# Kernel tuning notes

Hardware: AMD Instinct MI355X
Metric: run time of the kernel (lower is better)

## Reference

```python
import math
import jax, jax.numpy as jnp
import numpy as np

B, S, D_MODEL, N_HEADS, D_KV = 8, 1024, 1024, 16, 64
INNER = N_HEADS * D_KV
NUM_BUCKETS, MAX_DISTANCE = 32, 128


def _relative_position_bucket(relative_position, bidirectional=True,
                              num_buckets=NUM_BUCKETS, max_distance=MAX_DISTANCE):
    # Faithful port of T5Attention._relative_position_bucket (int math).
    relative_buckets = jnp.zeros_like(relative_position)
    if bidirectional:
        num_buckets //= 2
        relative_buckets += (relative_position > 0).astype(jnp.int32) * num_buckets
        relative_position = jnp.abs(relative_position)
    else:
        relative_position = -jnp.minimum(relative_position, 0)
    max_exact = num_buckets // 2
    is_small = relative_position < max_exact
    # clamp to >=1 before log to avoid -inf -> int cast (value unused when is_small)
    rp_f = jnp.maximum(relative_position, 1).astype(jnp.float32)
    rel_if_large = max_exact + (
        jnp.log(rp_f / max_exact) / math.log(max_distance / max_exact)
        * (num_buckets - max_exact)
    ).astype(jnp.int32)
    rel_if_large = jnp.minimum(rel_if_large, num_buckets - 1)
    relative_buckets += jnp.where(is_small, relative_position, rel_if_large)
    return relative_buckets


def compute_bias(rel_bias_emb, query_length, key_length):
    context_position = jnp.arange(query_length, dtype=jnp.int32)[:, None]
    memory_position = jnp.arange(key_length, dtype=jnp.int32)[None, :]
    relative_position = memory_position - context_position  # [Q, K]
    buckets = _relative_position_bucket(relative_position, bidirectional=True)
    values = rel_bias_emb[buckets]                 # [Q, K, H]
    return jnp.transpose(values, (2, 0, 1))[None]  # [1, H, Q, K]


def setup_inputs() -> dict:
    key = jax.random.key(0)
    k1, k2, k3, k4 = jax.random.split(key, 4)
    return {
        "hidden_states": jax.random.normal(k1, (B, S, D_MODEL), jnp.float32),
        "w_qkv": jax.random.normal(k2, (3 * INNER, D_MODEL), jnp.float32) * 0.02,
        "rel_bias_emb": jax.random.normal(k3, (NUM_BUCKETS, N_HEADS), jnp.float32) * 0.02,
        "w_out": jax.random.normal(k4, (D_MODEL, INNER), jnp.float32) * 0.02,
    }


def reference(hidden_states, w_qkv, rel_bias_emb, w_out):
    # QKV projection (no bias)
    qkv = jnp.einsum('bsd,ed->bse', hidden_states, w_qkv)  # [B,S,3*INNER]
    q, k, v = jnp.split(qkv, 3, axis=-1)
    q = q.reshape(B, S, N_HEADS, D_KV)
    k = k.reshape(B, S, N_HEADS, D_KV)
    v = v.reshape(B, S, N_HEADS, D_KV)
    # T5 attention uses scale = 1.0 (no 1/sqrt(d))
    scores = jnp.einsum('bqhd,bkhd->bhqk', q, k)           # [B,H,S,S]
    scores = scores + compute_bias(rel_bias_emb, S, S)     # additive rel-pos bias
    probs = jax.nn.softmax(scores, axis=-1)
    attn = jnp.einsum('bhqk,bkhd->bqhd', probs, v).reshape(B, S, INNER)
    return jnp.einsum('bsi,di->bsd', attn, w_out)          # out_proj, no bias
```

## Files before the change

### kernel.cpp

```cpp
#include <hip/hip_runtime.h>
#include <math.h>

typedef __attribute__((ext_vector_type(8))) short short8;
typedef __attribute__((ext_vector_type(4))) float f32x4;
typedef __attribute__((ext_vector_type(16))) float f32x16;
typedef __attribute__((ext_vector_type(4))) int int32x4;
typedef unsigned short bf16_t;

#define GLOAD_LDS16(g, l)                                                   \
    __builtin_amdgcn_global_load_lds(                                       \
        (__attribute__((address_space(1))) void*)(g),                       \
        (__attribute__((address_space(3))) void*)(l), 16, 0, 0)

__device__ __forceinline__ bf16_t f2b_rne(float f) {
    unsigned int u = __float_as_uint(f);
    u += 0x7FFFu + ((u >> 16) & 1u);
    return (bf16_t)(u >> 16);
}

__device__ __forceinline__ void store_out(bf16_t* p, float v) { *p = f2b_rne(v); }
__device__ __forceinline__ void store_out(float* p, float v) { *p = v; }

__global__ __launch_bounds__(256) void f2b_kernel(const float* __restrict__ in,
                                                  bf16_t* __restrict__ out, int n4) {
    int stride = gridDim.x * 256;
    for (int i = blockIdx.x * 256 + threadIdx.x; i < n4; i += stride) {
        float4 v = ((const float4*)in)[i];
        ushort4 p;
        p.x = f2b_rne(v.x); p.y = f2b_rne(v.y);
        p.z = f2b_rne(v.z); p.w = f2b_rne(v.w);
        ((ushort4*)out)[i] = p;
    }
}

__global__ void build_bias_tab(const float* __restrict__ emb, float* __restrict__ tab) {
    int idx = blockIdx.x * 256 + threadIdx.x;
    if (idx >= 2047) return;
    int rel = idx - 1023;
    int rb = rel > 0 ? 16 : 0;
    int rp = rel < 0 ? -rel : rel;
    int bucket;
    if (rp < 8) {
        bucket = rb + rp;
    } else {
        float t = logf((float)rp * 0.125f);
        int vi = 8 + (int)(t / 2.772588722239781f * 8.0f);
        bucket = rb + (vi < 15 ? vi : 15);
    }
    #pragma unroll
    for (int hh = 0; hh < 16; hh++)
        tab[hh * 2048 + idx] = emb[bucket * 16 + hh];
}

template <typename OT>
__global__ __launch_bounds__(256) void gemm_mfma(const bf16_t* __restrict__ A,
                                                 const bf16_t* __restrict__ B,
                                                 OT* __restrict__ C, int N, int gx) {
    __shared__ __align__(16) bf16_t As[128 * 32];
    __shared__ __align__(16) bf16_t Bs[128 * 32];
    const int nwg = gridDim.x;
    const int cpx = nwg >> 3;
    const int swz = (blockIdx.x & 7) * cpx + (blockIdx.x >> 3);
    const int bx = swz % gx, by = swz / gx;

    const int tid = threadIdx.x;
    const int lane = tid & 63;
    const int wv = tid >> 6;
    const int wr = wv >> 1, wc = wv & 1;
    const int m0 = by * 128, n0 = bx * 128;
    const int cc = lane & 15, cg = lane >> 4;

    f32x4 acc[4][4];
    #pragma unroll
    for (int i = 0; i < 4; i++)
        #pragma unroll
        for (int j = 0; j < 4; j++) acc[i][j] = {0.f, 0.f, 0.f, 0.f};

    for (int k0 = 0; k0 < 1024; k0 += 32) {
        __syncthreads();
        #pragma unroll
        for (int it = 0; it < 2; it++) {
            int c = it * 256 + tid;
            int r = c >> 2, kc = (c & 3) * 8;
            GLOAD_LDS16(A + (size_t)(m0 + r) * 1024 + k0 + kc, &As[c * 8]);
            GLOAD_LDS16(B + (size_t)(n0 + r) * 1024 + k0 + kc, &Bs[c * 8]);
        }
        __syncthreads();

        short8 af[4], bf[4];
        #pragma unroll
        for (int mf = 0; mf < 4; mf++)
            af[mf] = *(const short8*)&As[(wr * 64 + mf * 16 + cc) * 32 + cg * 8];
        #pragma unroll
        for (int nf = 0; nf < 4; nf++)
            bf[nf] = *(const short8*)&Bs[(wc * 64 + nf * 16 + cc) * 32 + cg * 8];
        #pragma unroll
        for (int mf = 0; mf < 4; mf++)
            #pragma unroll
            for (int nf = 0; nf < 4; nf++)
                acc[mf][nf] = __builtin_amdgcn_mfma_f32_16x16x32_bf16(
                    af[mf], bf[nf], acc[mf][nf], 0, 0, 0);
    }

    #pragma unroll
    for (int mf = 0; mf < 4; mf++)
        #pragma unroll
        for (int j = 0; j < 4; j++) {
            size_t row = (size_t)(m0 + wr * 64 + mf * 16 + cg * 4 + j);
            OT* cp = C + row * N + n0 + wc * 64 + cc;
            #pragma unroll
            for (int nf = 0; nf < 4; nf++) store_out(cp + nf * 16, acc[mf][nf][j]);
        }
}

__global__ __launch_bounds__(256) void relayout_k(const bf16_t* __restrict__ qkvb,
                                                  bf16_t* __restrict__ klin) {
    int gid = blockIdx.x * 256 + threadIdx.x;
    int lane = gid & 63;
    int s = (gid >> 6) & 3;
    int kt = (gid >> 8) & 31;
    int bh = gid >> 13;
    int b = bh >> 4, h = bh & 15;
    int key = kt * 32 + (lane & 31);
    int d0 = 16 * s + 8 * (lane >> 5);
    const bf16_t* src = qkvb + (size_t)(b * 1024 + key) * 3072 + 1024 + h * 64 + d0;
    *(short8*)(klin + (size_t)gid * 8) = *(const short8*)src;
}

__global__ __launch_bounds__(256) void relayout_v(const bf16_t* __restrict__ qkvb,
                                                  bf16_t* __restrict__ vt2) {
    int gid = blockIdx.x * 256 + threadIdx.x;
    int lane = gid & 63;
    int i = (gid >> 6) & 3;
    int kt = (gid >> 8) & 31;
    int bh = gid >> 13;
    int b = bh >> 4, h = bh & 15;
    int half = i >> 1, s2 = i & 1;
    int key0 = kt * 32 + 16 * s2 + 8 * (lane >> 5);
    int d = (lane & 31) + 32 * half;
    const bf16_t* src = qkvb + (size_t)(b * 1024 + key0) * 3072 + 2048 + h * 64 + d;
    short8 v;
    #pragma unroll
    for (int j = 0; j < 8; j++) v[j] = (short)src[(size_t)j * 3072];
    *(short8*)(vt2 + (size_t)gid * 8) = v;
}

__global__ __launch_bounds__(256, 3) void attn_mfma4(const bf16_t* __restrict__ qkv,
                                                     const float* __restrict__ tab,
                                                     const bf16_t* __restrict__ klin,
                                                     const bf16_t* __restrict__ vt2,
                                                     bf16_t* __restrict__ attn_out) {
    __shared__ float bias2[2304];
    __shared__ bf16_t Ol[4 * 32 * 68];

    const int i = blockIdx.x;
    const int g = ((i >> 6) << 3) + (i & 7);
    const int qc = (i >> 3) & 7;
    const int b = g >> 4, h = g & 15;
    const int q0 = qc * 128;

    const int tid = threadIdx.x;
    const int lane = tid & 63;
    const int w = tid >> 6;
    const int l31 = lane & 31;
    const int hi = lane >> 5;

    const float* tabh = tab + h * 2048;
    const int wbase = 896 - q0;
    #pragma unroll
    for (int it = 0; it < 5; it++) {
        int j = it * 256 + tid;
        if (j < 1151) {
            bias2[2 * j]     = tabh[wbase + j];
            bias2[2 * j + 1] = tabh[wbase + j + 1];
        }
    }

    const size_t rs = 3072;
    const bf16_t* Qg = qkv + (size_t)b * 1024 * rs + h * 64;
    const bf16_t* kl = klin + (size_t)g * 65536;
    const bf16_t* vl = vt2 + (size_t)g * 65536;

    const int qloc = w * 32 + l31;
    short8 qf[4];
    #pragma unroll
    for (int s = 0; s < 4; s++)
        qf[s] = *(const short8*)(Qg + (size_t)(q0 + qloc) * rs + 8 * hi + 16 * s);

    f32x16 O0 = (f32x16)0.f, O1 = (f32x16)0.f;
    float m_run = -1e30f, l_run = 0.f;

    auto loadk = [&](short8 (&dst)[4], int kt) {
        const bf16_t* kp = kl + (size_t)kt * 2048 + lane * 8;
        #pragma unroll
        for (int s = 0; s < 4; s++) dst[s] = *(const short8*)(kp + s * 512);
    };

    auto compute = [&](short8 (&kf)[4], int kt) {
        const int k0 = kt * 32;
        const bf16_t* vp = vl + (size_t)kt * 2048 + lane * 8;
        short8 vf0 = *(const short8*)vp;
        short8 vf1 = *(const short8*)(vp + 512);
        short8 vf2 = *(const short8*)(vp + 1024);
        short8 vf3 = *(const short8*)(vp + 1536);

        f32x16 S = (f32x16)0.f;
        #pragma unroll
        for (int s = 0; s < 4; s++)
            S = __builtin_amdgcn_mfma_f32_32x32x16_bf16(kf[s], qf[s], S, 0, 0, 0);

        float p[16];
        #pragma unroll
        for (int gg = 0; gg < 4; gg++) {
            int bi = k0 + 8 * gg + 4 * hi + 127 - qloc;
            float2 b0 = *(const float2*)&bias2[2 * bi];
            float2 b1 = *(const float2*)&bias2[2 * (bi + 2)];
            p[4 * gg + 0] = S[4 * gg + 0] + b0.x;
            p[4 * gg + 1] = S[4 * gg + 1] + b0.y;
            p[4 * gg + 2] = S[4 * gg + 2] + b1.x;
            p[4 * gg + 3] = S[4 * gg + 3] + b1.y;
        }

        float pmax = p[0];
        #pragma unroll
        for (int r = 1; r < 16; r++) pmax = fmaxf(pmax, p[r]);
        pmax = fmaxf(pmax, __shfl_xor(pmax, 32));
        if (!__all(pmax - m_run <= 8.f)) {
            float mn = fmaxf(m_run, pmax);
            float sc = __expf(m_run - mn);
            l_run *= sc;
            #pragma unroll
            for (int r = 0; r < 16; r++) { O0[r] *= sc; O1[r] *= sc; }
            m_run = mn;
        }
        float rsum = 0.f;
        #pragma unroll
        for (int r = 0; r < 16; r++) { p[r] = __expf(p[r] - m_run); rsum += p[r]; }
        rsum += __shfl_xor(rsum, 32);
        l_run += rsum;

        unsigned int wv[8];
        #pragma unroll
        for (int ii = 0; ii < 8; ii++) {
            unsigned int t;
            asm("v_cvt_pk_bf16_f32 %0, %1, %2" : "=v"(t) : "v"(p[2 * ii]), "v"(p[2 * ii + 1]));
            wv[ii] = t;
        }
        unsigned int x0 = __shfl_xor(hi ? wv[0] : wv[2], 32);
        unsigned int x1 = __shfl_xor(hi ? wv[1] : wv[3], 32);
        unsigned int x2 = __shfl_xor(hi ? wv[4] : wv[6], 32);
        unsigned int x3 = __shfl_xor(hi ? wv[5] : wv[7], 32);
        int32x4 pf0i, pf1i;
        if (hi) {
            pf0i = (int32x4){(int)x0, (int)x1, (int)wv[2], (int)wv[3]};
            pf1i = (int32x4){(int)x2, (int)x3, (int)wv[6], (int)wv[7]};
        } else {
            pf0i = (int32x4){(int)wv[0], (int)wv[1], (int)x0, (int)x1};
            pf1i = (int32x4){(int)wv[4], (int)wv[5], (int)x2, (int)x3};
        }
        short8 pf0 = __builtin_bit_cast(short8, pf0i);
        short8 pf1 = __builtin_bit_cast(short8, pf1i);

        O0 = __builtin_amdgcn_mfma_f32_32x32x16_bf16(vf0, pf0, O0, 0, 0, 0);
        O0 = __builtin_amdgcn_mfma_f32_32x32x16_bf16(vf1, pf1, O0, 0, 0, 0);
        O1 = __builtin_amdgcn_mfma_f32_32x32x16_bf16(vf2, pf0, O1, 0, 0, 0);
        O1 = __builtin_amdgcn_mfma_f32_32x32x16_bf16(vf3, pf1, O1, 0, 0, 0);
    };

    __syncthreads();

    short8 kA[4], kB[4];
    loadk(kA, 0);
    for (int kt = 0; kt < 32; kt += 2) {
        loadk(kB, kt + 1);
        compute(kA, kt);
        if (kt < 30) loadk(kA, kt + 2);
        compute(kB, kt + 1);
    }

    float inv = 1.f / l_run;
    bf16_t* olw = &Ol[w * 32 * 68];
    #pragma unroll
    for (int r = 0; r < 16; r++) {
        int dr = (r & 3) + 8 * (r >> 2) + 4 * hi;
        olw[l31 * 68 + dr]      = f2b_rne(O0[r] * inv);
        olw[l31 * 68 + dr + 32] = f2b_rne(O1[r] * inv);
    }
    bf16_t* outp = attn_out + (size_t)(b * 1024 + q0 + w * 32) * 1024 + h * 64;
    #pragma unroll 4
    for (int i2 = 0; i2 < 32; i2++)
        outp[(size_t)i2 * 1024 + lane] = olw[i2 * 68 + lane];
}

extern "C" void kernel_launch(void* const* d_in, const int* in_sizes, int n_in,
                              void* d_out, int out_size, void* d_ws, size_t ws_size,
                              hipStream_t stream) {
    const float* hs   = (const float*)d_in[0];
    const float* wqkv = (const float*)d_in[1];
    const float* emb  = (const float*)d_in[2];
    const float* wout = (const float*)d_in[3];
    float* out = (float*)d_out;

    char* p = (char*)d_ws;
    bf16_t* qkvb  = (bf16_t*)p; p += (size_t)8192 * 3072 * 2;
    bf16_t* attnb = (bf16_t*)p; p += (size_t)8192 * 1024 * 2;
    bf16_t* hsb   = (bf16_t*)p; p += (size_t)8192 * 1024 * 2;
    bf16_t* wqkvb = (bf16_t*)p; p += (size_t)3072 * 1024 * 2;
    bf16_t* woutb = (bf16_t*)p; p += (size_t)1024 * 1024 * 2;
    bf16_t* klin  = (bf16_t*)p; p += (size_t)128 * 65536 * 2;
    bf16_t* vt2   = (bf16_t*)p; p += (size_t)128 * 65536 * 2;
    float*  tab   = (float*)p;

    f2b_kernel<<<2048, 256, 0, stream>>>(hs, hsb, 8192 * 1024 / 4);
    f2b_kernel<<<768, 256, 0, stream>>>(wqkv, wqkvb, 3072 * 1024 / 4);
    f2b_kernel<<<256, 256, 0, stream>>>(wout, woutb, 1024 * 1024 / 4);
    build_bias_tab<<<8, 256, 0, stream>>>(emb, tab);

    gemm_mfma<bf16_t><<<1536, 256, 0, stream>>>(hsb, wqkvb, qkvb, 3072, 24);
    relayout_k<<<4096, 256, 0, stream>>>(qkvb, klin);
    relayout_v<<<4096, 256, 0, stream>>>(qkvb, vt2);
    attn_mfma4<<<1024, 256, 0, stream>>>(qkvb, tab, klin, vt2, attnb);
    gemm_mfma<float><<<512, 256, 0, stream>>>(attnb, woutb, out, 1024, 8);
}
```

Before: 258.5 us.

## Fuse QKV relayout into GEMM epilogue and swizzle GEMM LDS layout

The QKV projection GEMM now writes Q, K and V directly into the per-head MFMA-friendly tiled layouts, so the separate relayout_k/relayout_v kernels and the full qkv round trip through memory go away. Q is also pre-tiled, which lets the attention kernel load its fragments contiguously. Separately, GEMM LDS tiles get an XOR swizzle on the k-chunk to reduce bank conflicts on fragment reads. The fused epilogue issues scattered 2-byte stores, which may coalesce poorly.

```diff
diff --git a/kernel.cpp b/kernel.cpp
--- a/kernel.cpp
+++ b/kernel.cpp
@@ -17,9 +17,6 @@
     u += 0x7FFFu + ((u >> 16) & 1u);
     return (bf16_t)(u >> 16);
 }
-
-__device__ __forceinline__ void store_out(bf16_t* p, float v) { *p = f2b_rne(v); }
-__device__ __forceinline__ void store_out(float* p, float v) { *p = v; }
 
 __global__ __launch_bounds__(256) void f2b_kernel(const float* __restrict__ in,
                                                   bf16_t* __restrict__ out, int n4) {
@@ -52,10 +49,13 @@
         tab[hh * 2048 + idx] = emb[bucket * 16 + hh];
 }
 
-template <typename OT>
+template <int MODE, typename OT>
 __global__ __launch_bounds__(256) void gemm_mfma(const bf16_t* __restrict__ A,
                                                  const bf16_t* __restrict__ B,
-                                                 OT* __restrict__ C, int N, int gx) {
+                                                 OT* __restrict__ C, int N, int gx,
+                                                 bf16_t* __restrict__ qlin,
+                                                 bf16_t* __restrict__ klin,
+                                                 bf16_t* __restrict__ vlin) {
     __shared__ __align__(16) bf16_t As[128 * 32];
     __shared__ __align__(16) bf16_t Bs[128 * 32];
     const int nwg = gridDim.x;
@@ -76,12 +76,15 @@
         #pragma unroll
         for (int j = 0; j < 4; j++) acc[i][j] = {0.f, 0.f, 0.f, 0.f};
 
+    const int rsw = (cc >> 1) & 3;
+
     for (int k0 = 0; k0 < 1024; k0 += 32) {
         __syncthreads();
         #pragma unroll
         for (int it = 0; it < 2; it++) {
             int c = it * 256 + tid;
-            int r = c >> 2, kc = (c & 3) * 8;
+            int r = c >> 2, sl = c & 3;
+            int kc = (sl ^ ((r >> 1) & 3)) * 8;
             GLOAD_LDS16(A + (size_t)(m0 + r) * 1024 + k0 + kc, &As[c * 8]);
             GLOAD_LDS16(B + (size_t)(n0 + r) * 1024 + k0 + kc, &Bs[c * 8]);
         }
@@ -90,10 +93,10 @@
         short8 af[4], bf[4];
         #pragma unroll
         for (int mf = 0; mf < 4; mf++)
-            af[mf] = *(const short8*)&As[(wr * 64 + mf * 16 + cc) * 32 + cg * 8];
+            af[mf] = *(const short8*)&As[(wr * 64 + mf * 16 + cc) * 32 + (cg ^ rsw) * 8];
         #pragma unroll
         for (int nf = 0; nf < 4; nf++)
-            bf[nf] = *(const short8*)&Bs[(wc * 64 + nf * 16 + cc) * 32 + cg * 8];
+            bf[nf] = *(const short8*)&Bs[(wc * 64 + nf * 16 + cc) * 32 + (cg ^ rsw) * 8];
         #pragma unroll
         for (int mf = 0; mf < 4; mf++)
             #pragma unroll
@@ -102,53 +105,48 @@
                     af[mf], bf[nf], acc[mf][nf], 0, 0, 0);
     }
 
-    #pragma unroll
-    for (int mf = 0; mf < 4; mf++)
-        #pragma unroll
-        for (int j = 0; j < 4; j++) {
-            size_t row = (size_t)(m0 + wr * 64 + mf * 16 + cg * 4 + j);
-            OT* cp = C + row * N + n0 + wc * 64 + cc;
+    if constexpr (MODE == 0) {
+        #pragma unroll
+        for (int mf = 0; mf < 4; mf++)
             #pragma unroll
-            for (int nf = 0; nf < 4; nf++) store_out(cp + nf * 16, acc[mf][nf][j]);
-        }
-}
-
-__global__ __launch_bounds__(256) void relayout_k(const bf16_t* __restrict__ qkvb,
-                                                  bf16_t* __restrict__ klin) {
-    int gid = blockIdx.x * 256 + threadIdx.x;
-    int lane = gid & 63;
-    int s = (gid >> 6) & 3;
-    int kt = (gid >> 8) & 31;
-    int bh = gid >> 13;
-    int b = bh >> 4, h = bh & 15;
-    int key = kt * 32 + (lane & 31);
-    int d0 = 16 * s + 8 * (lane >> 5);
-    const bf16_t* src = qkvb + (size_t)(b * 1024 + key) * 3072 + 1024 + h * 64 + d0;
-    *(short8*)(klin + (size_t)gid * 8) = *(const short8*)src;
-}
-
-__global__ __launch_bounds__(256) void relayout_v(const bf16_t* __restrict__ qkvb,
-                                                  bf16_t* __restrict__ vt2) {
-    int gid = blockIdx.x * 256 + threadIdx.x;
-    int lane = gid & 63;
-    int i = (gid >> 6) & 3;
-    int kt = (gid >> 8) & 31;
-    int bh = gid >> 13;
-    int b = bh >> 4, h = bh & 15;
-    int half = i >> 1, s2 = i & 1;
-    int key0 = kt * 32 + 16 * s2 + 8 * (lane >> 5);
-    int d = (lane & 31) + 32 * half;
-    const bf16_t* src = qkvb + (size_t)(b * 1024 + key0) * 3072 + 2048 + h * 64 + d;
-    short8 v;
-    #pragma unroll
-    for (int j = 0; j < 8; j++) v[j] = (short)src[(size_t)j * 3072];
-    *(short8*)(vt2 + (size_t)gid * 8) = v;
-}
-
-__global__ __launch_bounds__(256, 3) void attn_mfma4(const bf16_t* __restrict__ qkv,
+            for (int j = 0; j < 4; j++) {
+                size_t row = (size_t)(m0 + wr * 64 + mf * 16 + cg * 4 + j);
+                OT* cp = C + row * N + n0 + wc * 64 + cc;
+                #pragma unroll
+                for (int nf = 0; nf < 4; nf++) cp[nf * 16] = acc[mf][nf][j];
+            }
+    } else {
+        const int part = n0 >> 10;
+        const int h = ((n0 + wc * 64) >> 6) & 15;
+        #pragma unroll
+        for (int mf = 0; mf < 4; mf++)
+            #pragma unroll
+            for (int j = 0; j < 4; j++) {
+                int row = m0 + wr * 64 + mf * 16 + cg * 4 + j;
+                int bi = row >> 10, seq = row & 1023;
+                size_t bh = (size_t)(bi * 16 + h);
+                #pragma unroll
+                for (int nf = 0; nf < 4; nf++) {
+                    int d = nf * 16 + cc;
+                    bf16_t v = f2b_rne(acc[mf][nf][j]);
+                    if (part == 2) {
+                        int lane16 = (d & 31) + 32 * ((seq >> 3) & 1);
+                        int ii = (d >> 5) * 2 + ((seq >> 4) & 1);
+                        vlin[(((bh * 32 + (seq >> 5)) * 4 + ii) * 64 + lane16) * 8 + (seq & 7)] = v;
+                    } else {
+                        int lane16 = (seq & 31) + 32 * ((d >> 3) & 1);
+                        bf16_t* dst = (part == 0) ? qlin : klin;
+                        dst[(((bh * 32 + (seq >> 5)) * 4 + (d >> 4)) * 64 + lane16) * 8 + (d & 7)] = v;
+                    }
+                }
+            }
+    }
+}
+
+__global__ __launch_bounds__(256, 3) void attn_mfma4(const bf16_t* __restrict__ qlin,
                                                      const float* __restrict__ tab,
                                                      const bf16_t* __restrict__ klin,
-                                                     const bf16_t* __restrict__ vt2,
+                                                     const bf16_t* __restrict__ vlin,
                                                      bf16_t* __restrict__ attn_out) {
     __shared__ float bias2[2304];
     __shared__ bf16_t Ol[4 * 32 * 68];
@@ -176,16 +174,16 @@
         }
     }
 
-    const size_t rs = 3072;
-    const bf16_t* Qg = qkv + (size_t)b * 1024 * rs + h * 64;
+    const bf16_t* ql = qlin + (size_t)g * 65536;
     const bf16_t* kl = klin + (size_t)g * 65536;
-    const bf16_t* vl = vt2 + (size_t)g * 65536;
+    const bf16_t* vl = vlin + (size_t)g * 65536;
 
     const int qloc = w * 32 + l31;
+    const int qt = qc * 4 + w;
     short8 qf[4];
     #pragma unroll
     for (int s = 0; s < 4; s++)
-        qf[s] = *(const short8*)(Qg + (size_t)(q0 + qloc) * rs + 8 * hi + 16 * s);
+        qf[s] = *(const short8*)(ql + (size_t)qt * 2048 + s * 512 + lane * 8);
 
     f32x16 O0 = (f32x16)0.f, O1 = (f32x16)0.f;
     float m_run = -1e30f, l_run = 0.f;
@@ -302,13 +300,13 @@
     float* out = (float*)d_out;
 
     char* p = (char*)d_ws;
-    bf16_t* qkvb  = (bf16_t*)p; p += (size_t)8192 * 3072 * 2;
-    bf16_t* attnb = (bf16_t*)p; p += (size_t)8192 * 1024 * 2;
     bf16_t* hsb   = (bf16_t*)p; p += (size_t)8192 * 1024 * 2;
     bf16_t* wqkvb = (bf16_t*)p; p += (size_t)3072 * 1024 * 2;
     bf16_t* woutb = (bf16_t*)p; p += (size_t)1024 * 1024 * 2;
+    bf16_t* qlin  = (bf16_t*)p; p += (size_t)128 * 65536 * 2;
     bf16_t* klin  = (bf16_t*)p; p += (size_t)128 * 65536 * 2;
-    bf16_t* vt2   = (bf16_t*)p; p += (size_t)128 * 65536 * 2;
+    bf16_t* vlin  = (bf16_t*)p; p += (size_t)128 * 65536 * 2;
+    bf16_t* attnb = (bf16_t*)p; p += (size_t)8192 * 1024 * 2;
     float*  tab   = (float*)p;
 
     f2b_kernel<<<2048, 256, 0, stream>>>(hs, hsb, 8192 * 1024 / 4);
@@ -316,9 +314,9 @@
     f2b_kernel<<<256, 256, 0, stream>>>(wout, woutb, 1024 * 1024 / 4);
     build_bias_tab<<<8, 256, 0, stream>>>(emb, tab);
 
-    gemm_mfma<bf16_t><<<1536, 256, 0, stream>>>(hsb, wqkvb, qkvb, 3072, 24);
-    relayout_k<<<4096, 256, 0, stream>>>(qkvb, klin);
-    relayout_v<<<4096, 256, 0, stream>>>(qkvb, vt2);
-    attn_mfma4<<<1024, 256, 0, stream>>>(qkvb, tab, klin, vt2, attnb);
-    gemm_mfma<float><<<512, 256, 0, stream>>>(attnb, woutb, out, 1024, 8);
-}
+    gemm_mfma<1, bf16_t><<<1536, 256, 0, stream>>>(hsb, wqkvb, (bf16_t*)nullptr, 3072, 24,
+                                                   qlin, klin, vlin);
+    attn_mfma4<<<1024, 256, 0, stream>>>(qlin, tab, klin, vlin, attnb);
+    gemm_mfma<0, float><<<512, 256, 0, stream>>>(attnb, woutb, out, 1024, 8,
+                                                 nullptr, nullptr, nullptr);
+}
```

Result: no change. 260.5 us (+0.8%).
